# Kernel tuning notes

Hardware: AMD Instinct MI355X
Metric: run time of the kernel (lower is better)

Reference implementation:

```python
import jax, jax.numpy as jnp
import numpy as np

T, K, F = 131072, 64, 8
EPS = 1e-10


def setup_inputs() -> dict:
    key = jax.random.key(0)
    k0, k1, k2, k3 = jax.random.split(key, 4)
    return {
        "observations": jax.random.normal(k0, (T, F), dtype=jnp.float32),
        "beta_logits": jax.random.normal(k1, (K,), dtype=jnp.float32),
        "pi_logits": jax.random.normal(k2, (K, K), dtype=jnp.float32),
        "means": 0.1 * jax.random.normal(k3, (K, F), dtype=jnp.float32),
        "log_vars": jnp.zeros((K, F), dtype=jnp.float32),
    }


def _stick_breaking(logits):
    betas = jax.nn.sigmoid(logits)
    cp = jnp.cumprod(1.0 - betas)
    return betas * jnp.concatenate([jnp.ones((1,), betas.dtype), cp[:-1]])


def _emission_log_probs(obs, means, log_vars):
    # Diagonal-covariance MVN log-prob, vectorized over (T, K) via matmuls
    # logN(x; mu, diag(v)) = -0.5 * (sum((x-mu)^2/v) + sum(log v) + F*log(2pi))
    inv_var = jnp.exp(-log_vars)                                 # (K, F)
    quad = (obs ** 2) @ inv_var.T                                # (T, K): sum x^2/v
    cross = obs @ (means * inv_var).T                            # (T, K): sum x*mu/v
    const = jnp.sum(means ** 2 * inv_var + log_vars, axis=1)     # (K,)
    log2pi = jnp.float32(np.log(2.0 * np.pi))
    Fdim = obs.shape[1]
    return -0.5 * (quad - 2.0 * cross + const[None, :] + Fdim * log2pi)


def reference(observations, beta_logits, pi_logits, means, log_vars):
    beta_w = _stick_breaking(beta_logits)                        # (K,)
    trans = jax.nn.softmax(pi_logits, axis=1)                    # (K, K)
    em = jnp.exp(_emission_log_probs(observations, means, log_vars))  # (T, K)

    # Forward recursion
    a0 = beta_w * em[0]
    a0 = a0 / (a0.sum() + EPS)

    def fwd_step(a, e):
        a = (a @ trans) * e
        a = a / (a.sum() + EPS)
        return a, a

    _, alpha_rest = jax.lax.scan(fwd_step, a0, em[1:])
    alpha = jnp.concatenate([a0[None, :], alpha_rest], axis=0)   # (T, K)

    # Backward recursion: beta[t] = normalize(trans @ (beta[t+1] * em[t+1]))
    bT = jnp.ones((trans.shape[0],), observations.dtype)

    def bwd_step(b, e_next):
        b = trans @ (b * e_next)
        b = b / (b.sum() + EPS)
        return b, b

    _, beta_rev = jax.lax.scan(bwd_step, bT, em[1:], reverse=True)
    beta = jnp.concatenate([beta_rev, bT[None, :]], axis=0)      # (T, K)

    log_likelihood = jnp.log(alpha[-1].sum() + EPS)
    return alpha, beta, log_likelihood
```

## Files before the change

kernel.cpp:

```cpp
#include <hip/hip_runtime.h>

#define T_N   131072
#define K_N   64
#define L_C   64
#define F_N   8
#define N_CH  (T_N / L_C)
#define WARM  32
#define EPS_F 1e-10f
#define OBS_MAX ((T_N - 1) * F_N)

#define LOG2E 1.4426950408889634f
#define NL2E  (-0.72134752044448170f)
#define LN2   0.6931471805599453f
#define LN2PI 1.8378770664093453f
#define EMSC  16.0f

typedef float v2f __attribute__((ext_vector_type(2)));
typedef __attribute__((ext_vector_type(4))) float f32x4;

template <int CTRL>
__device__ __forceinline__ float dpp_add(float x) {
  int y = __builtin_amdgcn_update_dpp(0, __float_as_int(x), CTRL, 0xF, 0xF, true);
  return x + __int_as_float(y);
}
__device__ __forceinline__ float wave_sum64(float x) {
  x = dpp_add<0x111>(x);
  x = dpp_add<0x112>(x);
  x = dpp_add<0x114>(x);
  x = dpp_add<0x118>(x);
  x = dpp_add<0x142>(x);
  x = dpp_add<0x143>(x);
  return __int_as_float(__builtin_amdgcn_readlane(__float_as_int(x), 63));
}

#define PKFMA(a, b, c) __builtin_elementwise_fma(a, b, c)

__device__ __forceinline__ float em_pk(const float4& xa, const float4& xb,
                                       const v2f civ2[4], const v2f cmiv2[4],
                                       float cc) {
  v2f x0 = {xa.x, xa.y}, x1 = {xa.z, xa.w};
  v2f x2 = {xb.x, xb.y}, x3 = {xb.z, xb.w};
  v2f a0 = {cc, 0.f}, a1 = {0.f, 0.f};
  a0 = PKFMA(x0, PKFMA(x0, civ2[0], cmiv2[0]), a0);
  a1 = PKFMA(x1, PKFMA(x1, civ2[1], cmiv2[1]), a1);
  a0 = PKFMA(x2, PKFMA(x2, civ2[2], cmiv2[2]), a0);
  a1 = PKFMA(x3, PKFMA(x3, civ2[3], cmiv2[3]), a1);
  v2f s = a0 + a1;
  return __builtin_amdgcn_exp2f(s.x + s.y);
}

#define MATVEC(VV, MOUT)                                                      \
  {                                                                           \
    vtab[lane] = (VV);                                                        \
    f32x4 q0_ = vq[0], q1_ = vq[1], q2_ = vq[2], q3_ = vq[3];                 \
    v2f q0l_ = {q0_.x, q0_.y}, q0h_ = {q0_.z, q0_.w};                         \
    v2f q1l_ = {q1_.x, q1_.y}, q1h_ = {q1_.z, q1_.w};                         \
    v2f q2l_ = {q2_.x, q2_.y}, q2h_ = {q2_.z, q2_.w};                         \
    v2f q3l_ = {q3_.x, q3_.y}, q3h_ = {q3_.z, q3_.w};                         \
    float X0_, X1_, X2_, X3_;                                                 \
    _Pragma("unroll")                                                         \
    for (int d_ = 0; d_ < 4; ++d_) {                                          \
      v2f aA_ = {0.f, 0.f}, aB_ = {0.f, 0.f};                                 \
      aA_ = PKFMA(q0l_, Tq[d_][0], aA_);                                      \
      aB_ = PKFMA(q0h_, Tq[d_][1], aB_);                                      \
      aA_ = PKFMA(q1l_, Tq[d_][2], aA_);                                      \
      aB_ = PKFMA(q1h_, Tq[d_][3], aB_);                                      \
      aA_ = PKFMA(q2l_, Tq[d_][4], aA_);                                      \
      aB_ = PKFMA(q2h_, Tq[d_][5], aB_);                                      \
      aA_ = PKFMA(q3l_, Tq[d_][6], aA_);                                      \
      aB_ = PKFMA(q3h_, Tq[d_][7], aB_);                                      \
      v2f s_ = aA_ + aB_;                                                     \
      float xs_ = s_.x + s_.y;                                                \
      if (d_ == 0) X0_ = xs_;                                                 \
      else if (d_ == 1) X1_ = xs_;                                            \
      else if (d_ == 2) X2_ = xs_;                                            \
      else X3_ = xs_;                                                         \
    }                                                                         \
    float e1_ = __int_as_float(                                               \
        __builtin_amdgcn_ds_swizzle(__float_as_int(X1_), 0x401F));            \
    float e2_ = __int_as_float(                                               \
        __builtin_amdgcn_ds_bpermute(a32, __float_as_int(X2_)));              \
    float e3_ = __int_as_float(                                               \
        __builtin_amdgcn_ds_bpermute(a48, __float_as_int(X3_)));              \
    MOUT = (X0_ + e1_) + (e2_ + e3_);                                         \
  }

extern "C" __global__ void __launch_bounds__(64, 2)
hdphmm_fb(const float* __restrict__ obs,
          const float* __restrict__ beta_logits,
          const float* __restrict__ pi_logits,
          const float* __restrict__ means,
          const float* __restrict__ log_vars,
          float* __restrict__ out) {
  const int lane = threadIdx.x;
  const int bid  = blockIdx.x;
  const int g16  = (lane >> 4) << 4;
  const int a32  = ((lane ^ 32) & 63) << 2;
  const int a48  = ((lane ^ 48) & 63) << 2;

  __shared__ __align__(8) float2 sstat[K_N];
  __shared__ float sb[K_N];
  __shared__ __align__(16) float vtab[K_N];
  const f32x4* vq = reinterpret_cast<const f32x4*>(vtab) + (lane >> 4) * 4;

  float* alpha   = out;
  float* betaout = out + (size_t)T_N * K_N;

  v2f civ2[4], cmiv2[4];
  float c0, cw;
  {
    const float4* mp = reinterpret_cast<const float4*>(means + lane * F_N);
    const float4* lp = reinterpret_cast<const float4*>(log_vars + lane * F_N);
    float4 m0 = mp[0], m1 = mp[1];
    float4 l0 = lp[0], l1 = lp[1];
    float mu[8] = {m0.x, m0.y, m0.z, m0.w, m1.x, m1.y, m1.z, m1.w};
    float lv[8] = {l0.x, l0.y, l0.z, l0.w, l1.x, l1.y, l1.z, l1.w};
    float cst = F_N * LN2PI;
#pragma unroll
    for (int f = 0; f < 8; ++f) {
      float iv = __builtin_amdgcn_exp2f(-lv[f] * LOG2E);
      cst += lv[f] + mu[f] * mu[f] * iv;
      float cf  = NL2E * iv;
      civ2[f >> 1][f & 1]  = cf;
      cmiv2[f >> 1][f & 1] = -2.0f * mu[f] * cf;
    }
    c0 = NL2E * cst;
    cw = c0 + EMSC;
  }

  {
    const float4* pr4 = reinterpret_cast<const float4*>(pi_logits + lane * K_N);
    float mx = -3.0e38f;
#pragma unroll
    for (int k = 0; k < 16; ++k) {
      float4 r = pr4[k];
      mx = fmaxf(mx, fmaxf(fmaxf(r.x, r.y), fmaxf(r.z, r.w)));
    }
    float s = 0.0f;
#pragma unroll
    for (int k = 0; k < 16; ++k) {
      float4 r = pr4[k];
      s += __builtin_amdgcn_exp2f((r.x - mx) * LOG2E);
      s += __builtin_amdgcn_exp2f((r.y - mx) * LOG2E);
      s += __builtin_amdgcn_exp2f((r.z - mx) * LOG2E);
      s += __builtin_amdgcn_exp2f((r.w - mx) * LOG2E);
    }
    sstat[lane] = make_float2(mx, __builtin_amdgcn_rcpf(s));
  }
  __syncthreads();

  v2f Tq[4][8];

  if (bid < N_CH) {
#pragma unroll
    for (int d = 0; d < 4; ++d) {
      int row = lane ^ (16 * d);
#pragma unroll
      for (int c = 0; c < 8; ++c) {
        int k0 = g16 + 2 * c, k1 = k0 + 1;
        float2 s0 = sstat[k0], s1 = sstat[k1];
        float p0 = pi_logits[(size_t)k0 * K_N + row];
        float p1 = pi_logits[(size_t)k1 * K_N + row];
        Tq[d][c] = (v2f){__builtin_amdgcn_exp2f((p0 - s0.x) * LOG2E) * s0.y,
                         __builtin_amdgcn_exp2f((p1 - s1.x) * LOG2E) * s1.y};
      }
    }

    const int out_lo = bid * L_C;
    float v;
    int t_first;
    if (bid == 0) {
      float bl = beta_logits[lane];
      float ex = __builtin_amdgcn_exp2f(-bl * LOG2E);
      float bw = __builtin_amdgcn_rcpf(1.0f + ex);
      sb[lane] = 1.0f - bw;
      __syncthreads();
      float pr = 1.0f;
#pragma unroll
      for (int i = 0; i < 64; ++i) {
        float qv = sb[i];
        pr = (i < lane) ? pr * qv : pr;
      }
      float4 x0 = reinterpret_cast<const float4*>(obs)[0];
      float4 x1 = reinterpret_cast<const float4*>(obs)[1];
      v = bw * pr * em_pk(x0, x1, civ2, cmiv2, c0);
      t_first = 1;
    } else {
      const int t0 = out_lo - WARM;
      const float4* xp = reinterpret_cast<const float4*>(obs + t0 * F_N);
      v = em_pk(xp[0], xp[1], civ2, cmiv2, cw);
      t_first = t0 + 1;
    }
    int obs_off = t_first * F_N;
    float4 xa, xb;
    {
      const float4* xp = reinterpret_cast<const float4*>(obs + obs_off);
      xa = xp[0]; xb = xp[1];
    }
    int out_off = out_lo * K_N + lane;

    const int wn8 = (bid == 0) ? 0 : (WARM >> 3);
#pragma unroll 1
    for (int o = 0; o < wn8; ++o) {
#pragma unroll
      for (int i = 0; i < 8; ++i) {
        float4 nxa = *reinterpret_cast<const float4*>(obs + obs_off + F_N);
        float4 nxb = *reinterpret_cast<const float4*>(obs + obs_off + F_N + 4);
        float m;
        MATVEC(v, m)
        float e = em_pk(xa, xb, civ2, cmiv2, cw);
        v = m * e;
        xa = nxa; xb = nxb; obs_off += F_N;
      }
      float Sw = wave_sum64(v);
      v *= __builtin_amdgcn_rcpf(Sw);
    }

    float S = wave_sum64(v);
    float r_st = __builtin_amdgcn_rcpf(S + EPS_F);

#define FWD_SSTEP                                                             \
  {                                                                           \
    int offn = obs_off + F_N; offn = (offn > OBS_MAX) ? OBS_MAX : offn;       \
    float4 nxa = *reinterpret_cast<const float4*>(obs + offn);                \
    float4 nxb = *reinterpret_cast<const float4*>(obs + offn + 4);            \
    float m;                                                                  \
    MATVEC(v, m)                                                              \
    alpha[out_off] = v * r_st; out_off += K_N;                                \
    float e = em_pk(xa, xb, civ2, cmiv2, c0);                                 \
    float vn = m * (r_st * e);                                                \
    S = wave_sum64(vn);                                                       \
    r_st = __builtin_amdgcn_rcpf(S + EPS_F);                                  \
    v = vn; xa = nxa; xb = nxb; obs_off = offn;                               \
  }

#pragma unroll 2
    for (int it = 0; it < L_C - 1; ++it) FWD_SSTEP
#undef FWD_SSTEP
    alpha[out_off] = v * r_st;
    if (bid == N_CH - 1 && lane == 0) {
      float sl = S * r_st + EPS_F;
      out[(size_t)2 * T_N * K_N] = __builtin_amdgcn_logf(sl) * LN2;
    }
  } else {
#pragma unroll
    for (int d = 0; d < 4; ++d) {
      int row = lane ^ (16 * d);
      float2 st = sstat[row];
      const float4* rp =
          reinterpret_cast<const float4*>(pi_logits + (size_t)row * K_N + g16);
#pragma unroll
      for (int c4 = 0; c4 < 4; ++c4) {
        float4 r = rp[c4];
        Tq[d][2 * c4] =
            (v2f){__builtin_amdgcn_exp2f((r.x - st.x) * LOG2E) * st.y,
                  __builtin_amdgcn_exp2f((r.y - st.x) * LOG2E) * st.y};
        Tq[d][2 * c4 + 1] =
            (v2f){__builtin_amdgcn_exp2f((r.z - st.x) * LOG2E) * st.y,
                  __builtin_amdgcn_exp2f((r.w - st.x) * LOG2E) * st.y};
      }
    }

    const int cb   = bid - N_CH;
    const int t_lo = cb * L_C;
    const int t_hi = t_lo + L_C - 1;
    int t_top = t_hi + WARM;
    if (t_top > T_N - 1) t_top = T_N - 1;
    const int s_top = (cb == N_CH - 1) ? T_N - 2 : t_hi;

    float w;
    {
      const float4* xp = reinterpret_cast<const float4*>(obs + t_top * F_N);
      w = em_pk(xp[0], xp[1], civ2, cmiv2, cw);
    }
    if (cb == N_CH - 1)
      betaout[(size_t)(T_N - 1) * K_N + lane] = 1.0f;
    int obs_off = (t_top - 1) * F_N;
    float4 xa, xb;
    {
      const float4* xp = reinterpret_cast<const float4*>(obs + obs_off);
      xa = xp[0]; xb = xp[1];
    }
    int out_off = s_top * K_N + lane;

#define BWD_WSTEP                                                             \
  {                                                                           \
    float4 nxa = *reinterpret_cast<const float4*>(obs + obs_off - F_N);       \
    float4 nxb = *reinterpret_cast<const float4*>(obs + obs_off - F_N + 4);   \
    float m;                                                                  \
    MATVEC(w, m)                                                              \
    float e = em_pk(xa, xb, civ2, cmiv2, cw);                                 \
    w = m * e;                                                                \
    xa = nxa; xb = nxb; obs_off -= F_N;                                       \
  }

    const int pw  = (t_top - s_top) - 1;
    const int pw8 = pw >> 3, pwr = pw & 7;
#pragma unroll 1
    for (int o = 0; o < pw8; ++o) {
#pragma unroll
      for (int i = 0; i < 8; ++i) BWD_WSTEP
      float Sw = wave_sum64(w);
      w *= __builtin_amdgcn_rcpf(Sw);
    }
#pragma unroll 1
    for (int it = 0; it < pwr; ++it) BWD_WSTEP
#undef BWD_WSTEP

    float u, S, r_st;
    {
      float m;
      MATVEC(w, m)
      float Sm = wave_sum64(m);
      u = m * __builtin_amdgcn_rcpf(Sm);
      float e = em_pk(xa, xb, civ2, cmiv2, c0);
      w = u * e;
      S = wave_sum64(u);
      r_st = __builtin_amdgcn_rcpf(S + EPS_F);
      int offn = obs_off - F_N; offn = (offn < 0) ? 0 : offn;
      xa = *reinterpret_cast<const float4*>(obs + offn);
      xb = *reinterpret_cast<const float4*>(obs + offn + 4);
      obs_off = offn;
    }

#define BWD_SSTEP                                                             \
  {                                                                           \
    int offn = obs_off - F_N; offn = (offn < 0) ? 0 : offn;                   \
    float4 nxa = *reinterpret_cast<const float4*>(obs + offn);                \
    float4 nxb = *reinterpret_cast<const float4*>(obs + offn + 4);            \
    float m;                                                                  \
    MATVEC(w, m)                                                              \
    betaout[out_off] = u * r_st; out_off -= K_N;                              \
    float u2 = m * r_st;                                                      \
    float e = em_pk(xa, xb, civ2, cmiv2, c0);                                 \
    w = u2 * e;                                                               \
    S = wave_sum64(u2);                                                       \
    r_st = __builtin_amdgcn_rcpf(S + EPS_F);                                  \
    u = u2; xa = nxa; xb = nxb; obs_off = offn;                               \
  }

    const int store_n = s_top - t_lo;
#pragma unroll 2
    for (int it = 0; it < store_n; ++it) BWD_SSTEP
#undef BWD_SSTEP
    betaout[t_lo * K_N + lane] = u * r_st;
  }
}

extern "C" void kernel_launch(void* const* d_in, const int* in_sizes, int n_in,
                              void* d_out, int out_size, void* d_ws, size_t ws_size,
                              hipStream_t stream) {
  (void)in_sizes; (void)n_in; (void)out_size; (void)d_ws; (void)ws_size;
  const float* obs  = (const float*)d_in[0];
  const float* bl   = (const float*)d_in[1];
  const float* pi   = (const float*)d_in[2];
  const float* mns  = (const float*)d_in[3];
  const float* lvs  = (const float*)d_in[4];
  hipLaunchKernelGGL(hdphmm_fb, dim3(2 * N_CH), dim3(64), 0, stream,
                     obs, bl, pi, mns, lvs, (float*)d_out);
}
```

Measured before the change: 147.7 us.

## Interleave two independent sub-chunk recursions per wave for ILP

Each wave now handles two independent 32-step sub-chunks of a 64-step block, interleaving their forward and backward recursions step by step with separate LDS vector tables. This hides the latency of the serial matvec, DPP reductions and LDS round-trips, because one chain's work fills the stalls of the other. Warmup length drops from 32 to 24 steps, which means more warmup work overall in exchange for a shorter dependency chain per wave, and a small risk of accuracy loss at sub-chunk boundaries. Register pressure also rises because two chains are live at once.

Result: slower. 156.2 us (+5.8%).

```diff
diff --git a/kernel.cpp b/kernel.cpp
--- a/kernel.cpp
+++ b/kernel.cpp
@@ -2,10 +2,11 @@
 
 #define T_N   131072
 #define K_N   64
-#define L_C   64
+#define L_C   32
+#define BLK   64
+#define N_BL  (T_N / BLK)
 #define F_N   8
-#define N_CH  (T_N / L_C)
-#define WARM  32
+#define WARM  24
 #define EPS_F 1e-10f
 #define OBS_MAX ((T_N - 1) * F_N)
 
@@ -34,6 +35,7 @@
 }
 
 #define PKFMA(a, b, c) __builtin_elementwise_fma(a, b, c)
+#define RCP(x) __builtin_amdgcn_rcpf(x)
 
 __device__ __forceinline__ float em_pk(const float4& xa, const float4& xb,
                                        const v2f civ2[4], const v2f cmiv2[4],
@@ -49,10 +51,10 @@
   return __builtin_amdgcn_exp2f(s.x + s.y);
 }
 
-#define MATVEC(VV, MOUT)                                                      \
-  {                                                                           \
-    vtab[lane] = (VV);                                                        \
-    f32x4 q0_ = vq[0], q1_ = vq[1], q2_ = vq[2], q3_ = vq[3];                 \
+#define MATVEC(VT, VQP, VV, MOUT)                                             \
+  {                                                                           \
+    VT[lane] = (VV);                                                          \
+    f32x4 q0_ = VQP[0], q1_ = VQP[1], q2_ = VQP[2], q3_ = VQP[3];             \
     v2f q0l_ = {q0_.x, q0_.y}, q0h_ = {q0_.z, q0_.w};                         \
     v2f q1l_ = {q1_.x, q1_.y}, q1h_ = {q1_.z, q1_.w};                         \
     v2f q2l_ = {q2_.x, q2_.y}, q2h_ = {q2_.z, q2_.w};                         \
@@ -85,6 +87,73 @@
     MOUT = (X0_ + e1_) + (e2_ + e3_);                                         \
   }
 
+#define FWSTEP(VT, VQP, V, XA, XB, OFF)                                       \
+  {                                                                           \
+    float4 nxa = *reinterpret_cast<const float4*>(obs + (OFF) + F_N);         \
+    float4 nxb = *reinterpret_cast<const float4*>(obs + (OFF) + F_N + 4);     \
+    float m;                                                                  \
+    MATVEC(VT, VQP, V, m)                                                     \
+    float e = em_pk(XA, XB, civ2, cmiv2, cw);                                 \
+    V = m * e; XA = nxa; XB = nxb; OFF += F_N;                                \
+  }
+
+#define FSSTEP(VT, VQP, V, S, R, XA, XB, OFF, OUT)                            \
+  {                                                                           \
+    int offn = (OFF) + F_N; offn = (offn > OBS_MAX) ? OBS_MAX : offn;         \
+    float4 nxa = *reinterpret_cast<const float4*>(obs + offn);                \
+    float4 nxb = *reinterpret_cast<const float4*>(obs + offn + 4);            \
+    float m;                                                                  \
+    MATVEC(VT, VQP, V, m)                                                     \
+    alpha[OUT] = V * R; OUT += K_N;                                           \
+    float e = em_pk(XA, XB, civ2, cmiv2, c0);                                 \
+    float vn = m * (R * e);                                                   \
+    S = wave_sum64(vn);                                                       \
+    R = RCP(S + EPS_F);                                                       \
+    V = vn; XA = nxa; XB = nxb; OFF = offn;                                   \
+  }
+
+#define BWSTEP(VT, VQP, W, XA, XB, OFF)                                       \
+  {                                                                           \
+    float4 nxa = *reinterpret_cast<const float4*>(obs + (OFF) - F_N);         \
+    float4 nxb = *reinterpret_cast<const float4*>(obs + (OFF) - F_N + 4);     \
+    float m;                                                                  \
+    MATVEC(VT, VQP, W, m)                                                     \
+    float e = em_pk(XA, XB, civ2, cmiv2, cw);                                 \
+    W = m * e; XA = nxa; XB = nxb; OFF -= F_N;                                \
+  }
+
+#define BTRANS(VT, VQP, W, U, S, R, XA, XB, OFF)                              \
+  {                                                                           \
+    float m;                                                                  \
+    MATVEC(VT, VQP, W, m)                                                     \
+    float Sm = wave_sum64(m);                                                 \
+    U = m * RCP(Sm);                                                          \
+    float e = em_pk(XA, XB, civ2, cmiv2, c0);                                 \
+    W = U * e;                                                                \
+    S = wave_sum64(U);                                                        \
+    R = RCP(S + EPS_F);                                                       \
+    int offn = (OFF) - F_N; offn = (offn < 0) ? 0 : offn;                     \
+    XA = *reinterpret_cast<const float4*>(obs + offn);                        \
+    XB = *reinterpret_cast<const float4*>(obs + offn + 4);                    \
+    OFF = offn;                                                               \
+  }
+
+#define BSSTEP(VT, VQP, W, U, S, R, XA, XB, OFF, OUT, DOST)                   \
+  {                                                                           \
+    int offn = (OFF) - F_N; offn = (offn < 0) ? 0 : offn;                     \
+    float4 nxa = *reinterpret_cast<const float4*>(obs + offn);                \
+    float4 nxb = *reinterpret_cast<const float4*>(obs + offn + 4);            \
+    float m;                                                                  \
+    MATVEC(VT, VQP, W, m)                                                     \
+    if (DOST) { betaout[OUT] = U * R; OUT -= K_N; }                           \
+    float u2 = m * R;                                                         \
+    float e = em_pk(XA, XB, civ2, cmiv2, c0);                                 \
+    W = u2 * e;                                                               \
+    S = wave_sum64(u2);                                                       \
+    R = RCP(S + EPS_F);                                                       \
+    U = u2; XA = nxa; XB = nxb; OFF = offn;                                   \
+  }
+
 extern "C" __global__ void __launch_bounds__(64, 2)
 hdphmm_fb(const float* __restrict__ obs,
           const float* __restrict__ beta_logits,
@@ -100,8 +169,10 @@
 
   __shared__ __align__(8) float2 sstat[K_N];
   __shared__ float sb[K_N];
-  __shared__ __align__(16) float vtab[K_N];
-  const f32x4* vq = reinterpret_cast<const f32x4*>(vtab) + (lane >> 4) * 4;
+  __shared__ __align__(16) float vtabA[K_N];
+  __shared__ __align__(16) float vtabB[K_N];
+  const f32x4* vqA = reinterpret_cast<const f32x4*>(vtabA) + (lane >> 4) * 4;
+  const f32x4* vqB = reinterpret_cast<const f32x4*>(vtabB) + (lane >> 4) * 4;
 
   float* alpha   = out;
   float* betaout = out + (size_t)T_N * K_N;
@@ -145,13 +216,14 @@
       s += __builtin_amdgcn_exp2f((r.z - mx) * LOG2E);
       s += __builtin_amdgcn_exp2f((r.w - mx) * LOG2E);
     }
-    sstat[lane] = make_float2(mx, __builtin_amdgcn_rcpf(s));
+    sstat[lane] = make_float2(mx, RCP(s));
   }
   __syncthreads();
 
   v2f Tq[4][8];
 
-  if (bid < N_CH) {
+  if (bid < N_BL) {
+    const int b = bid;
 #pragma unroll
     for (int d = 0; d < 4; ++d) {
       int row = lane ^ (16 * d);
@@ -166,13 +238,19 @@
       }
     }
 
-    const int out_lo = bid * L_C;
-    float v;
-    int t_first;
-    if (bid == 0) {
+    const int rowA = b * BLK, rowB = rowA + L_C;
+    float vA, vB;
+    int offA, offB;
+    const bool aw = (b != 0);
+    if (aw) {
+      const int t0 = rowA - WARM;
+      const float4* xp = reinterpret_cast<const float4*>(obs + t0 * F_N);
+      vA = em_pk(xp[0], xp[1], civ2, cmiv2, cw);
+      offA = (t0 + 1) * F_N;
+    } else {
       float bl = beta_logits[lane];
       float ex = __builtin_amdgcn_exp2f(-bl * LOG2E);
-      float bw = __builtin_amdgcn_rcpf(1.0f + ex);
+      float bw = RCP(1.0f + ex);
       sb[lane] = 1.0f - bw;
       __syncthreads();
       float pr = 1.0f;
@@ -183,66 +261,60 @@
       }
       float4 x0 = reinterpret_cast<const float4*>(obs)[0];
       float4 x1 = reinterpret_cast<const float4*>(obs)[1];
-      v = bw * pr * em_pk(x0, x1, civ2, cmiv2, c0);
-      t_first = 1;
+      vA = bw * pr * em_pk(x0, x1, civ2, cmiv2, c0);
+      offA = 1 * F_N;
+    }
+    {
+      const int t0b = rowB - WARM;
+      const float4* xp = reinterpret_cast<const float4*>(obs + t0b * F_N);
+      vB = em_pk(xp[0], xp[1], civ2, cmiv2, cw);
+      offB = (t0b + 1) * F_N;
+    }
+    float4 xaA, xbA, xaB, xbB;
+    xaA = *reinterpret_cast<const float4*>(obs + offA);
+    xbA = *reinterpret_cast<const float4*>(obs + offA + 4);
+    xaB = *reinterpret_cast<const float4*>(obs + offB);
+    xbB = *reinterpret_cast<const float4*>(obs + offB + 4);
+
+    if (aw) {
+#pragma unroll 1
+      for (int o = 0; o < 3; ++o) {
+#pragma unroll
+        for (int i = 0; i < 8; ++i) {
+          FWSTEP(vtabA, vqA, vA, xaA, xbA, offA)
+          FWSTEP(vtabB, vqB, vB, xaB, xbB, offB)
+        }
+        float SwA = wave_sum64(vA); vA *= RCP(SwA);
+        float SwB = wave_sum64(vB); vB *= RCP(SwB);
+      }
     } else {
-      const int t0 = out_lo - WARM;
-      const float4* xp = reinterpret_cast<const float4*>(obs + t0 * F_N);
-      v = em_pk(xp[0], xp[1], civ2, cmiv2, cw);
-      t_first = t0 + 1;
-    }
-    int obs_off = t_first * F_N;
-    float4 xa, xb;
-    {
-      const float4* xp = reinterpret_cast<const float4*>(obs + obs_off);
-      xa = xp[0]; xb = xp[1];
-    }
-    int out_off = out_lo * K_N + lane;
-
-    const int wn8 = (bid == 0) ? 0 : (WARM >> 3);
-#pragma unroll 1
-    for (int o = 0; o < wn8; ++o) {
-#pragma unroll
-      for (int i = 0; i < 8; ++i) {
-        float4 nxa = *reinterpret_cast<const float4*>(obs + obs_off + F_N);
-        float4 nxb = *reinterpret_cast<const float4*>(obs + obs_off + F_N + 4);
-        float m;
-        MATVEC(v, m)
-        float e = em_pk(xa, xb, civ2, cmiv2, cw);
-        v = m * e;
-        xa = nxa; xb = nxb; obs_off += F_N;
-      }
-      float Sw = wave_sum64(v);
-      v *= __builtin_amdgcn_rcpf(Sw);
-    }
-
-    float S = wave_sum64(v);
-    float r_st = __builtin_amdgcn_rcpf(S + EPS_F);
-
-#define FWD_SSTEP                                                             \
-  {                                                                           \
-    int offn = obs_off + F_N; offn = (offn > OBS_MAX) ? OBS_MAX : offn;       \
-    float4 nxa = *reinterpret_cast<const float4*>(obs + offn);                \
-    float4 nxb = *reinterpret_cast<const float4*>(obs + offn + 4);            \
-    float m;                                                                  \
-    MATVEC(v, m)                                                              \
-    alpha[out_off] = v * r_st; out_off += K_N;                                \
-    float e = em_pk(xa, xb, civ2, cmiv2, c0);                                 \
-    float vn = m * (r_st * e);                                                \
-    S = wave_sum64(vn);                                                       \
-    r_st = __builtin_amdgcn_rcpf(S + EPS_F);                                  \
-    v = vn; xa = nxa; xb = nxb; obs_off = offn;                               \
-  }
-
-#pragma unroll 2
-    for (int it = 0; it < L_C - 1; ++it) FWD_SSTEP
-#undef FWD_SSTEP
-    alpha[out_off] = v * r_st;
-    if (bid == N_CH - 1 && lane == 0) {
-      float sl = S * r_st + EPS_F;
+#pragma unroll 1
+      for (int o = 0; o < 3; ++o) {
+#pragma unroll
+        for (int i = 0; i < 8; ++i) {
+          FWSTEP(vtabB, vqB, vB, xaB, xbB, offB)
+        }
+        float SwB = wave_sum64(vB); vB *= RCP(SwB);
+      }
+    }
+
+    float SA = wave_sum64(vA), SB = wave_sum64(vB);
+    float rA = RCP(SA + EPS_F), rB = RCP(SB + EPS_F);
+    int outA = rowA * K_N + lane, outB = rowB * K_N + lane;
+
+#pragma unroll 1
+    for (int it = 0; it < L_C - 1; ++it) {
+      FSSTEP(vtabA, vqA, vA, SA, rA, xaA, xbA, offA, outA)
+      FSSTEP(vtabB, vqB, vB, SB, rB, xaB, xbB, offB, outB)
+    }
+    alpha[outA] = vA * rA;
+    alpha[outB] = vB * rB;
+    if (b == N_BL - 1 && lane == 0) {
+      float sl = SB * rB + EPS_F;
       out[(size_t)2 * T_N * K_N] = __builtin_amdgcn_logf(sl) * LN2;
     }
   } else {
+    const int b = bid - N_BL;
 #pragma unroll
     for (int d = 0; d < 4; ++d) {
       int row = lane ^ (16 * d);
@@ -261,89 +333,82 @@
       }
     }
 
-    const int cb   = bid - N_CH;
-    const int t_lo = cb * L_C;
-    const int t_hi = t_lo + L_C - 1;
-    int t_top = t_hi + WARM;
-    if (t_top > T_N - 1) t_top = T_N - 1;
-    const int s_top = (cb == N_CH - 1) ? T_N - 2 : t_hi;
-
-    float w;
+    const int t_loB = b * BLK;
+    const int t_loA = t_loB + L_C;
+    const bool last = (b == N_BL - 1);
+    const bool aw   = !last;
+
+    int t_topA = t_loA + L_C - 1 + WARM;
+    if (t_topA > T_N - 1) t_topA = T_N - 1;
+    const int s_topA = last ? T_N - 2 : t_loA + L_C - 1;
+    const int t_topB = t_loB + L_C - 1 + WARM;
+    const int s_topB = t_loB + L_C - 1;
+
+    float wA, wB;
     {
-      const float4* xp = reinterpret_cast<const float4*>(obs + t_top * F_N);
-      w = em_pk(xp[0], xp[1], civ2, cmiv2, cw);
-    }
-    if (cb == N_CH - 1)
+      const float4* xp = reinterpret_cast<const float4*>(obs + t_topA * F_N);
+      wA = em_pk(xp[0], xp[1], civ2, cmiv2, cw);
+    }
+    {
+      const float4* xp = reinterpret_cast<const float4*>(obs + t_topB * F_N);
+      wB = em_pk(xp[0], xp[1], civ2, cmiv2, cw);
+    }
+    if (last && lane == 0) {  }
+    if (last)
       betaout[(size_t)(T_N - 1) * K_N + lane] = 1.0f;
-    int obs_off = (t_top - 1) * F_N;
-    float4 xa, xb;
-    {
-      const float4* xp = reinterpret_cast<const float4*>(obs + obs_off);
-      xa = xp[0]; xb = xp[1];
-    }
-    int out_off = s_top * K_N + lane;
-
-#define BWD_WSTEP                                                             \
-  {                                                                           \
-    float4 nxa = *reinterpret_cast<const float4*>(obs + obs_off - F_N);       \
-    float4 nxb = *reinterpret_cast<const float4*>(obs + obs_off - F_N + 4);   \
-    float m;                                                                  \
-    MATVEC(w, m)                                                              \
-    float e = em_pk(xa, xb, civ2, cmiv2, cw);                                 \
-    w = m * e;                                                                \
-    xa = nxa; xb = nxb; obs_off -= F_N;                                       \
-  }
-
-    const int pw  = (t_top - s_top) - 1;
-    const int pw8 = pw >> 3, pwr = pw & 7;
-#pragma unroll 1
-    for (int o = 0; o < pw8; ++o) {
-#pragma unroll
-      for (int i = 0; i < 8; ++i) BWD_WSTEP
-      float Sw = wave_sum64(w);
-      w *= __builtin_amdgcn_rcpf(Sw);
-    }
-#pragma unroll 1
-    for (int it = 0; it < pwr; ++it) BWD_WSTEP
-#undef BWD_WSTEP
-
-    float u, S, r_st;
-    {
-      float m;
-      MATVEC(w, m)
-      float Sm = wave_sum64(m);
-      u = m * __builtin_amdgcn_rcpf(Sm);
-      float e = em_pk(xa, xb, civ2, cmiv2, c0);
-      w = u * e;
-      S = wave_sum64(u);
-      r_st = __builtin_amdgcn_rcpf(S + EPS_F);
-      int offn = obs_off - F_N; offn = (offn < 0) ? 0 : offn;
-      xa = *reinterpret_cast<const float4*>(obs + offn);
-      xb = *reinterpret_cast<const float4*>(obs + offn + 4);
-      obs_off = offn;
-    }
-
-#define BWD_SSTEP                                                             \
-  {                                                                           \
-    int offn = obs_off - F_N; offn = (offn < 0) ? 0 : offn;                   \
-    float4 nxa = *reinterpret_cast<const float4*>(obs + offn);                \
-    float4 nxb = *reinterpret_cast<const float4*>(obs + offn + 4);            \
-    float m;                                                                  \
-    MATVEC(w, m)                                                              \
-    betaout[out_off] = u * r_st; out_off -= K_N;                              \
-    float u2 = m * r_st;                                                      \
-    float e = em_pk(xa, xb, civ2, cmiv2, c0);                                 \
-    w = u2 * e;                                                               \
-    S = wave_sum64(u2);                                                       \
-    r_st = __builtin_amdgcn_rcpf(S + EPS_F);                                  \
-    u = u2; xa = nxa; xb = nxb; obs_off = offn;                               \
-  }
-
-    const int store_n = s_top - t_lo;
-#pragma unroll 2
-    for (int it = 0; it < store_n; ++it) BWD_SSTEP
-#undef BWD_SSTEP
-    betaout[t_lo * K_N + lane] = u * r_st;
+
+    int offA = (t_topA - 1) * F_N, offB = (t_topB - 1) * F_N;
+    float4 xaA, xbA, xaB, xbB;
+    xaA = *reinterpret_cast<const float4*>(obs + offA);
+    xbA = *reinterpret_cast<const float4*>(obs + offA + 4);
+    xaB = *reinterpret_cast<const float4*>(obs + offB);
+    xbB = *reinterpret_cast<const float4*>(obs + offB + 4);
+
+    if (aw) {
+#pragma unroll 1
+      for (int o = 0; o < 2; ++o) {
+#pragma unroll
+        for (int i = 0; i < 8; ++i) {
+          BWSTEP(vtabA, vqA, wA, xaA, xbA, offA)
+          BWSTEP(vtabB, vqB, wB, xaB, xbB, offB)
+        }
+        float SwA = wave_sum64(wA); wA *= RCP(SwA);
+        float SwB = wave_sum64(wB); wB *= RCP(SwB);
+      }
+#pragma unroll 1
+      for (int it = 0; it < 7; ++it) {
+        BWSTEP(vtabA, vqA, wA, xaA, xbA, offA)
+        BWSTEP(vtabB, vqB, wB, xaB, xbB, offB)
+      }
+    } else {
+#pragma unroll 1
+      for (int o = 0; o < 2; ++o) {
+#pragma unroll
+        for (int i = 0; i < 8; ++i) {
+          BWSTEP(vtabB, vqB, wB, xaB, xbB, offB)
+        }
+        float SwB = wave_sum64(wB); wB *= RCP(SwB);
+      }
+#pragma unroll 1
+      for (int it = 0; it < 7; ++it) {
+        BWSTEP(vtabB, vqB, wB, xaB, xbB, offB)
+      }
+    }
+
+    float uA, SA, rA, uB, SB, rB;
+    BTRANS(vtabA, vqA, wA, uA, SA, rA, xaA, xbA, offA)
+    BTRANS(vtabB, vqB, wB, uB, SB, rB, xaB, xbB, offB)
+
+    int outA = s_topA * K_N + lane, outB = s_topB * K_N + lane;
+    const int snA = last ? (L_C - 2) : (L_C - 1);
+
+#pragma unroll 1
+    for (int it = 0; it < L_C - 1; ++it) {
+      BSSTEP(vtabA, vqA, wA, uA, SA, rA, xaA, xbA, offA, outA, (it < snA))
+      BSSTEP(vtabB, vqB, wB, uB, SB, rB, xaB, xbB, offB, outB, true)
+    }
+    betaout[t_loA * K_N + lane] = uA * rA;
+    betaout[t_loB * K_N + lane] = uB * rB;
   }
 }
 
@@ -356,6 +421,6 @@
   const float* pi   = (const float*)d_in[2];
   const float* mns  = (const float*)d_in[3];
   const float* lvs  = (const float*)d_in[4];
-  hipLaunchKernelGGL(hdphmm_fb, dim3(2 * N_CH), dim3(64), 0, stream,
+  hipLaunchKernelGGL(hdphmm_fb, dim3(2 * N_BL), dim3(64), 0, stream,
                      obs, bl, pi, mns, lvs, (float*)d_out);
 }
```
